# Optimization experiments

Hardware: AMD Instinct MI355X
Metric: run time of the kernel (lower is better)

The kernel has to match this reference:

```python
import jax, jax.numpy as jnp
import numpy as np

NH = 8      # num_heads
NP_ = 4     # num_points

def setup_inputs() -> dict:
    key = jax.random.key(0)
    ks = jax.random.split(key, 12)
    B, N, C = 8, 4096, 256
    query = jax.random.normal(ks[0], (B, N, C), jnp.float32)
    value = jax.random.normal(ks[1], (B, N, C), jnp.float32)
    reference_points = jax.random.uniform(ks[2], (B, N, 2), jnp.float32)
    xav = lambda k, i, o: jax.random.normal(k, (i, o), jnp.float32) * np.sqrt(2.0 / (i + o)).astype(np.float32)
    W_off = jax.random.normal(ks[3], (C, NH * NP_ * 2), jnp.float32) * 0.02  # small offsets (orig inits to 0)
    b_off = jax.random.normal(ks[4], (NH * NP_ * 2,), jnp.float32) * 0.02
    W_attn = xav(ks[5], C, NH * NP_)
    b_attn = jnp.zeros((NH * NP_,), jnp.float32)
    W_val = xav(ks[6], C, C)
    b_val = jnp.zeros((C,), jnp.float32)
    W_out = xav(ks[7], C, C)
    b_out = jnp.zeros((C,), jnp.float32)
    return dict(query=query, value=value, reference_points=reference_points,
                W_off=W_off, b_off=b_off, W_attn=W_attn, b_attn=b_attn,
                W_val=W_val, b_val=b_val, W_out=W_out, b_out=b_out)

def _deform_attn(query, value, reference_points, W_off, b_off, W_attn, b_attn, W_val, b_val, W_out, b_out):
    B, N, C = query.shape
    HW = value.shape[1]
    H = W = int(np.sqrt(HW))  # static
    hd = C // NH
    # value projection -> [B, NH, H*W, hd]
    vals = (value @ W_val + b_val).reshape(B, H, W, NH, hd)
    vals = vals.transpose(0, 3, 1, 2, 4).reshape(B, NH, H * W, hd)
    # offsets [B,N,NH,P,2] in [-0.5,0.5]; attention weights softmax over P
    off = jnp.tanh((query @ W_off + b_off).reshape(B, N, NH, NP_, 2)) * 0.5
    attn = jax.nn.softmax((query @ W_attn + b_attn).reshape(B, N, NH, NP_), axis=-1)
    # sampling locations in [0,1], then grid coords in [-1,1] (x=width, y=height)
    loc = jnp.clip(reference_points[:, :, None, None, :] + off, 0.0, 1.0)
    g = loc * 2.0 - 1.0
    # torch grid_sample, align_corners=False: pixel = (g+1)*size/2 - 0.5
    x = (g[..., 0] + 1.0) * (W * 0.5) - 0.5
    y = (g[..., 1] + 1.0) * (H * 0.5) - 0.5
    x0f = jnp.floor(x); y0f = jnp.floor(y)
    wx1 = x - x0f; wx0 = 1.0 - wx1
    wy1 = y - y0f; wy0 = 1.0 - wy1
    x0 = x0f.astype(jnp.int32); x1 = x0 + 1
    y0 = y0f.astype(jnp.int32); y1 = y0 + 1

    def corner(xi, yi, w):  # xi,yi,w: [B,N,NH,P]; zero padding outside
        valid = (xi >= 0) & (xi < W) & (yi >= 0) & (yi < H)
        idx = jnp.clip(yi, 0, H - 1) * W + jnp.clip(xi, 0, W - 1)
        idx_h = idx.transpose(0, 2, 1, 3).reshape(B, NH, N * NP_)      # [B,NH,N*P]
        gat = jnp.take_along_axis(vals, idx_h[..., None], axis=2)      # [B,NH,N*P,hd]
        wv = jnp.where(valid, w, 0.0).transpose(0, 2, 1, 3).reshape(B, NH, N * NP_)
        return gat * wv[..., None]

    sampled = (corner(x0, y0, wx0 * wy0) + corner(x1, y0, wx1 * wy0)
               + corner(x0, y1, wx0 * wy1) + corner(x1, y1, wx1 * wy1))
    sampled = sampled.reshape(B, NH, N, NP_, hd)
    attn_h = attn.transpose(0, 2, 1, 3)                                 # [B,NH,N,P]
    out = jnp.einsum('bhnpd,bhnp->bnhd', sampled, attn_h).reshape(B, N, C)
    return out @ W_out + b_out  # dropout is identity in eval

def reference(query, value, reference_points, W_off, b_off, W_attn, b_attn, W_val, b_val, W_out, b_out):
    return _deform_attn(query, value, reference_points, W_off, b_off, W_attn, b_attn, W_val, b_val, W_out, b_out)
```

## Files before the change

### kernel.cpp

```cpp
#include <hip/hip_runtime.h>
#include <math.h>

#define NHEAD 8
#define NPT 4
#define HDIM 32
#define IMG 64
#define CDIM 256
#define NQ 4096
#define BATCH 8
#define MTOT (BATCH * NQ)

typedef __attribute__((ext_vector_type(8))) short bf16x8;
typedef __attribute__((ext_vector_type(4))) float f32x4;

__device__ __forceinline__ unsigned short f2b(float f) {
    union { float f; unsigned u; } v; v.f = f;
    unsigned r = (v.u + 0x7FFFu + ((v.u >> 16) & 1u)) >> 16;
    return (unsigned short)r;
}
__device__ __forceinline__ float b2f(unsigned short u) {
    union { unsigned u; float f; } v; v.u = ((unsigned)u) << 16;
    return v.f;
}

#define SWZ(row, col)   ((col) ^ (((row) & 7) << 3))

__device__ __forceinline__ void gload16(const void* src, void* ldsbase) {
    __builtin_amdgcn_global_load_lds(
        (const __attribute__((address_space(1))) void*)src,
        (__attribute__((address_space(3))) void*)ldsbase, 16, 0, 0);
}


__global__ __launch_bounds__(256)
void cvt_weights_kernel(const float* __restrict__ Wv, const float* __restrict__ Wo,
                        const float* __restrict__ Woff, const float* __restrict__ Wattn,
                        const float* __restrict__ boff, const float* __restrict__ battn,
                        unsigned short* __restrict__ Wv_t, unsigned short* __restrict__ Wo_t,
                        unsigned short* __restrict__ Wl_h, unsigned short* __restrict__ Wl_l,
                        float* __restrict__ bias_lin)
{
    int tid = blockIdx.x * 256 + threadIdx.x;
    int n = tid & 255, k = tid >> 8;
    Wv_t[n * 256 + k] = f2b(Wv[k * 256 + n]);
    Wo_t[n * 256 + k] = f2b(Wo[k * 256 + n]);
    if (tid < 128 * 256) {
        int nn = tid >> 8;
        int kk = tid & 255;
        float v = (nn < 64) ? Woff[kk * 64 + nn]
                : (nn < 96) ? Wattn[kk * 32 + (nn - 64)] : 0.f;
        unsigned short hi = f2b(v);
        unsigned short lo = f2b(v - b2f(hi));
        Wl_h[nn * 256 + kk] = hi;
        Wl_l[nn * 256 + kk] = lo;
    }
    if (tid < 128)
        bias_lin[tid] = (tid < 64) ? boff[tid] : (tid < 96) ? battn[tid - 64] : 0.f;
}

__global__ __launch_bounds__(256)
void fused_gemms_kernel(const float* __restrict__ value,
                        const float* __restrict__ query,
                        const unsigned short* __restrict__ Wv_t,
                        const unsigned short* __restrict__ Wl_h,
                        const unsigned short* __restrict__ Wl_l,
                        const float* __restrict__ b_val,
                        unsigned short* __restrict__ projv,
                        float* __restrict__ lin)
{
    __shared__ __align__(16) char smem[32768];

    const int tid  = threadIdx.x;
    const int lane = tid & 63;
    const int wid  = tid >> 6;
    const int wr = (wid >> 1) * 64;
    const int wc = (wid & 1) * 64;
    const int l15 = lane & 15;
    const int lk  = (lane >> 4) * 8;

    const int b = blockIdx.x & 7;
    const int j = blockIdx.x >> 3;

    f32x4 acc[4][4];
    #pragma unroll
    for (int m = 0; m < 4; ++m)
        #pragma unroll
        for (int n = 0; n < 4; ++n)
            #pragma unroll
            for (int r = 0; r < 4; ++r) acc[m][n][r] = 0.f;

    if (j < 64) {
        unsigned short (*As)[64] = (unsigned short(*)[64])smem;
        unsigned short (*Bs)[64] = (unsigned short(*)[64])(smem + 16384);
        const int gm = (b << 12) + ((j & 31) << 7);
        const int gn = (j >> 5) << 7;
        const int rl  = lane >> 3;
        const int ch  = (lane & 7) ^ rl;

        for (int k0 = 0; k0 < 256; k0 += 64) {
            #pragma unroll
            for (int it = 0; it < 4; ++it) {
                const int br = it * 32 + wid * 8;
                gload16(&Wv_t[(size_t)(gn + br + rl) * 256 + k0 + ch * 8], &Bs[br][0]);
            }
            #pragma unroll
            for (int it = 0; it < 4; ++it) {
                const int chunk = it * 256 + tid;
                const int row = chunk >> 3;
                const int kc  = (chunk & 7) << 3;
                const float4* src = (const float4*)&value[(size_t)(gm + row) * 256 + k0 + kc];
                const float4 a = src[0], bb = src[1];
                float f[8] = {a.x, a.y, a.z, a.w, bb.x, bb.y, bb.z, bb.w};
                unsigned short h[8];
                #pragma unroll
                for (int jj = 0; jj < 8; ++jj) h[jj] = f2b(f[jj]);
                *(uint4*)&As[row][SWZ(row, kc)] = *(const uint4*)h;
            }
            __syncthreads();

            #pragma unroll
            for (int kk = 0; kk < 64; kk += 32) {
                bf16x8 a[4], bv[4];
                #pragma unroll
                for (int m = 0; m < 4; ++m) {
                    const int r = wr + m * 16 + l15;
                    a[m] = *(const bf16x8*)&As[r][SWZ(r, kk + lk)];
                }
                #pragma unroll
                for (int n = 0; n < 4; ++n) {
                    const int r = wc + n * 16 + l15;
                    bv[n] = *(const bf16x8*)&Bs[r][SWZ(r, kk + lk)];
                }
                #pragma unroll
                for (int m = 0; m < 4; ++m)
                    #pragma unroll
                    for (int n = 0; n < 4; ++n)
                        acc[m][n] = __builtin_amdgcn_mfma_f32_16x16x32_bf16(a[m], bv[n], acc[m][n], 0, 0, 0);
            }
            __syncthreads();
        }

        const int cr = (lane >> 4) * 4;
        #pragma unroll
        for (int n = 0; n < 4; ++n) {
            const int col = gn + wc + n * 16 + l15;
            const float bvv = b_val[col];
            #pragma unroll
            for (int m = 0; m < 4; ++m)
                #pragma unroll
                for (int r = 0; r < 4; ++r) {
                    const int row = gm + wr + m * 16 + cr + r;
                    projv[(size_t)row * 256 + col] = f2b(acc[m][n][r] + bvv);
                }
        }
    } else {
        float (*Aq)[32] = (float(*)[32])smem;
        unsigned short (*Bh)[32] = (unsigned short(*)[32])(smem + 16384);
        unsigned short (*Bl)[32] = (unsigned short(*)[32])(smem + 24576);
        const int u  = j - 64;
        const int gm = (b << 12) + ((u & 31) << 7);
        const int kq = u >> 5;
        const int rla = lane >> 3;
        const int ca  = (lane & 7) ^ rla;
        const int rsb = lane >> 2;
        const int cb  = (lane & 3) ^ (rsb & 3);

        for (int k0 = kq * 128; k0 < kq * 128 + 128; k0 += 32) {
            #pragma unroll
            for (int i = 0; i < 4; ++i) {
                const int ar = wid * 32 + i * 8;
                gload16(&query[(size_t)(gm + ar + rla) * 256 + k0 + ca * 4], &Aq[ar][0]);
            }
            #pragma unroll
            for (int i = 0; i < 2; ++i) {
                const int br = wid * 32 + i * 16;
                gload16(&Wl_h[(size_t)(br + rsb) * 256 + k0 + cb * 8], &Bh[br][0]);
                gload16(&Wl_l[(size_t)(br + rsb) * 256 + k0 + cb * 8], &Bl[br][0]);
            }
            __syncthreads();

            bf16x8 ah[4], al[4];
            #pragma unroll
            for (int m = 0; m < 4; ++m) {
                const int r = wr + m * 16 + l15;
                const int c0 = ((lk >> 2) ^ (r & 7)) << 2;
                const int c1 = (((lk >> 2) + 1) ^ (r & 7)) << 2;
                const f32x4 qa = *(const f32x4*)&Aq[r][c0];
                const f32x4 qb = *(const f32x4*)&Aq[r][c1];
                float f[8] = {qa.x, qa.y, qa.z, qa.w, qb.x, qb.y, qb.z, qb.w};
                unsigned short h[8], l[8];
                #pragma unroll
                for (int jj = 0; jj < 8; ++jj) {
                    h[jj] = f2b(f[jj]);
                    l[jj] = f2b(f[jj] - b2f(h[jj]));
                }
                ah[m] = *(const bf16x8*)h;
                al[m] = *(const bf16x8*)l;
            }

            const int nN = (wc == 0) ? 4 : 2;
            #pragma unroll
            for (int n = 0; n < 4; ++n) {
                if (n >= nN) break;
                const int r = wc + n * 16 + l15;
                const int c = ((lk >> 3) ^ (r & 3)) << 3;
                const bf16x8 bh = *(const bf16x8*)&Bh[r][c];
                const bf16x8 bl = *(const bf16x8*)&Bl[r][c];
                #pragma unroll
                for (int m = 0; m < 4; ++m) {
                    acc[m][n] = __builtin_amdgcn_mfma_f32_16x16x32_bf16(ah[m], bh, acc[m][n], 0, 0, 0);
                    acc[m][n] = __builtin_amdgcn_mfma_f32_16x16x32_bf16(ah[m], bl, acc[m][n], 0, 0, 0);
                    acc[m][n] = __builtin_amdgcn_mfma_f32_16x16x32_bf16(al[m], bh, acc[m][n], 0, 0, 0);
                }
            }
            __syncthreads();
        }

        float* dst = lin + (size_t)kq * MTOT * 96;
        const int cr = (lane >> 4) * 4;
        #pragma unroll
        for (int n = 0; n < 4; ++n) {
            const int col = wc + n * 16 + l15;
            if (col < 96) {
                #pragma unroll
                for (int m = 0; m < 4; ++m)
                    #pragma unroll
                    for (int r = 0; r < 4; ++r) {
                        const int row = gm + wr + m * 16 + cr + r;
                        dst[(size_t)row * 96 + col] = acc[m][n][r];
                    }
            }
        }
    }
}

__global__ __launch_bounds__(256)
void gemm_out_kernel(const unsigned short* __restrict__ Ap,
                     const unsigned short* __restrict__ Bt,
                     const float* __restrict__ bias,
                     float* __restrict__ C)
{
    __shared__ unsigned short As[128][64];
    __shared__ unsigned short Bs[128][64];

    const int tid  = threadIdx.x;
    const int lane = tid & 63;
    const int wid  = tid >> 6;
    const int gm = ((blockIdx.x & 7) << 12) + ((blockIdx.x >> 3) << 7);
    const int gn = blockIdx.y * 128;
    const int wr = (wid >> 1) * 64;
    const int wc = (wid & 1) * 64;
    const int l15 = lane & 15;
    const int lk  = (lane >> 4) * 8;
    const int rl  = lane >> 3;
    const int ch  = (lane & 7) ^ rl;

    f32x4 acc[4][4];
    #pragma unroll
    for (int m = 0; m < 4; ++m)
        #pragma unroll
        for (int n = 0; n < 4; ++n)
            #pragma unroll
            for (int r = 0; r < 4; ++r) acc[m][n][r] = 0.f;

    for (int k0 = 0; k0 < 256; k0 += 64) {
        #pragma unroll
        for (int it = 0; it < 4; ++it) {
            const int br = it * 32 + wid * 8;
            gload16(&Bt[(size_t)(gn + br + rl) * 256 + k0 + ch * 8], &Bs[br][0]);
            gload16(&Ap[(size_t)(gm + br + rl) * 256 + k0 + ch * 8], &As[br][0]);
        }
        __syncthreads();

        #pragma unroll
        for (int kk = 0; kk < 64; kk += 32) {
            bf16x8 a[4], b[4];
            #pragma unroll
            for (int m = 0; m < 4; ++m) {
                const int r = wr + m * 16 + l15;
                a[m] = *(const bf16x8*)&As[r][SWZ(r, kk + lk)];
            }
            #pragma unroll
            for (int n = 0; n < 4; ++n) {
                const int r = wc + n * 16 + l15;
                b[n] = *(const bf16x8*)&Bs[r][SWZ(r, kk + lk)];
            }
            #pragma unroll
            for (int m = 0; m < 4; ++m)
                #pragma unroll
                for (int n = 0; n < 4; ++n)
                    acc[m][n] = __builtin_amdgcn_mfma_f32_16x16x32_bf16(a[m], b[n], acc[m][n], 0, 0, 0);
        }
        __syncthreads();
    }

    const int cr = (lane >> 4) * 4;
    #pragma unroll
    for (int n = 0; n < 4; ++n) {
        const int col = gn + wc + n * 16 + l15;
        const float bv = bias[col];
        #pragma unroll
        for (int m = 0; m < 4; ++m)
            #pragma unroll
            for (int r = 0; r < 4; ++r) {
                const int row = gm + wr + m * 16 + cr + r;
                C[(size_t)row * 256 + col] = acc[m][n][r] + bv;
            }
    }
}

__global__ __launch_bounds__(256)
void sample_gather_kernel(const unsigned short* __restrict__ projv,
                          const float* __restrict__ lin,
                          const float* __restrict__ bias_lin,
                          const float* __restrict__ refp,
                          unsigned short* __restrict__ sampled)
{
    __shared__ float4 s_w[8][32];
    __shared__ unsigned s_xy[8][32];

    const int i = blockIdx.x;
    const int b = i & 7;
    const int bn0 = (b << 12) + ((i >> 3) << 3);
    const int t = threadIdx.x;

    {
        const int sub = t >> 5;
        const int q = t & 31;
        const int h = q >> 2;
        const int p = q & 3;
        const int bn = bn0 + sub;
        const float2 rp = *(const float2*)&refp[(size_t)bn * 2];
        const size_t base0 = (size_t)bn * 96;
        const size_t base1 = (size_t)MTOT * 96 + base0;
        const float2 o0 = *(const float2*)&lin[base0 + h * 8 + p * 2];
        const float2 o1 = *(const float2*)&lin[base1 + h * 8 + p * 2];
        const float2 ob = *(const float2*)&bias_lin[h * 8 + p * 2];
        const float olx = o0.x + o1.x + ob.x;
        const float oly = o0.y + o1.y + ob.y;
        const float al  = lin[base0 + 64 + q] + lin[base1 + 64 + q] + bias_lin[64 + q];

        float mx = al;
        mx = fmaxf(mx, __shfl_xor(mx, 1));
        mx = fmaxf(mx, __shfl_xor(mx, 2));
        float e = expf(al - mx);
        float s = e;
        s += __shfl_xor(s, 1);
        s += __shfl_xor(s, 2);
        const float aw = e / s;

        const float lx = fminf(fmaxf(rp.x + tanhf(olx) * 0.5f, 0.f), 1.f);
        const float ly = fminf(fmaxf(rp.y + tanhf(oly) * 0.5f, 0.f), 1.f);
        const float x = lx * (float)IMG - 0.5f;
        const float y = ly * (float)IMG - 0.5f;
        const float x0f = floorf(x), y0f = floorf(y);
        const int x0 = (int)x0f, y0 = (int)y0f;
        const float wx1 = x - x0f, wx0 = 1.f - wx1;
        const float wy1 = y - y0f, wy0 = 1.f - wy1;
        const bool vx0 = (x0 >= 0), vx1 = (x0 + 1 < IMG);
        const bool vy0 = (y0 >= 0), vy1 = (y0 + 1 < IMG);
        float4 w;
        w.x = (vx0 && vy0) ? wx0 * wy0 * aw : 0.f;
        w.y = (vx1 && vy0) ? wx1 * wy0 * aw : 0.f;
        w.z = (vx0 && vy1) ? wx0 * wy1 * aw : 0.f;
        w.w = (vx1 && vy1) ? wx1 * wy1 * aw : 0.f;
        const int x0c = min(max(x0, 0), IMG - 1), x1c = min(max(x0 + 1, 0), IMG - 1);
        const int y0c = min(max(y0, 0), IMG - 1), y1c = min(max(y0 + 1, 0), IMG - 1);
        s_w[sub][q] = w;
        s_xy[sub][q] = (unsigned)x0c | ((unsigned)x1c << 8) | ((unsigned)y0c << 16) | ((unsigned)y1c << 24);
    }
    __syncthreads();

    const int l = t & 63;
    const int h2 = l >> 3;
    const int cp = l & 7;
    const unsigned short* vbase = projv + ((size_t)b << 20) + h2 * HDIM + cp * 4;

    #pragma unroll
    for (int pass = 0; pass < 2; ++pass) {
        const int sub = (t >> 6) + pass * 4;
        const int bn = bn0 + sub;

        float a0 = 0.f, a1 = 0.f, a2 = 0.f, a3 = 0.f;
        #pragma unroll
        for (int p = 0; p < 4; ++p) {
            const float4 w = s_w[sub][h2 * 4 + p];
            const unsigned xy = s_xy[sub][h2 * 4 + p];
            const int x0 = xy & 255, x1 = (xy >> 8) & 255;
            const int y0 = (xy >> 16) & 255, y1 = xy >> 24;
            const uint2 u00 = *(const uint2*)&vbase[(((y0 << 6) + x0) << 8)];
            const uint2 u01 = *(const uint2*)&vbase[(((y0 << 6) + x1) << 8)];
            const uint2 u10 = *(const uint2*)&vbase[(((y1 << 6) + x0) << 8)];
            const uint2 u11 = *(const uint2*)&vbase[(((y1 << 6) + x1) << 8)];
            a0 += w.x * b2f((unsigned short)(u00.x & 0xffff)) + w.y * b2f((unsigned short)(u01.x & 0xffff))
                + w.z * b2f((unsigned short)(u10.x & 0xffff)) + w.w * b2f((unsigned short)(u11.x & 0xffff));
            a1 += w.x * b2f((unsigned short)(u00.x >> 16)) + w.y * b2f((unsigned short)(u01.x >> 16))
                + w.z * b2f((unsigned short)(u10.x >> 16)) + w.w * b2f((unsigned short)(u11.x >> 16));
            a2 += w.x * b2f((unsigned short)(u00.y & 0xffff)) + w.y * b2f((unsigned short)(u01.y & 0xffff))
                + w.z * b2f((unsigned short)(u10.y & 0xffff)) + w.w * b2f((unsigned short)(u11.y & 0xffff));
            a3 += w.x * b2f((unsigned short)(u00.y >> 16)) + w.y * b2f((unsigned short)(u01.y >> 16))
                + w.z * b2f((unsigned short)(u10.y >> 16)) + w.w * b2f((unsigned short)(u11.y >> 16));
        }
        uint2 outp;
        outp.x = (unsigned)f2b(a0) | ((unsigned)f2b(a1) << 16);
        outp.y = (unsigned)f2b(a2) | ((unsigned)f2b(a3) << 16);
        *(uint2*)&sampled[(size_t)bn * 256 + h2 * HDIM + cp * 4] = outp;
    }
}

extern "C" void kernel_launch(void* const* d_in, const int* in_sizes, int n_in,
                              void* d_out, int out_size, void* d_ws, size_t ws_size,
                              hipStream_t stream)
{
    const float* query  = (const float*)d_in[0];
    const float* value  = (const float*)d_in[1];
    const float* refp   = (const float*)d_in[2];
    const float* W_off  = (const float*)d_in[3];
    const float* b_off  = (const float*)d_in[4];
    const float* W_attn = (const float*)d_in[5];
    const float* b_attn = (const float*)d_in[6];
    const float* W_val  = (const float*)d_in[7];
    const float* b_val  = (const float*)d_in[8];
    const float* W_out  = (const float*)d_in[9];
    const float* b_out  = (const float*)d_in[10];
    float* out = (float*)d_out;

    char* ws = (char*)d_ws;
    unsigned short* projv    = (unsigned short*)ws; ws += (size_t)MTOT * 256 * 2;
    unsigned short* sampled  = (unsigned short*)ws; ws += (size_t)MTOT * 256 * 2;
    float*          lin      = (float*)ws;          ws += (size_t)2 * MTOT * 96 * 4;
    unsigned short* Wv_t     = (unsigned short*)ws; ws += 256 * 256 * 2;
    unsigned short* Wo_t     = (unsigned short*)ws; ws += 256 * 256 * 2;
    unsigned short* Wl_h     = (unsigned short*)ws; ws += 128 * 256 * 2;
    unsigned short* Wl_l     = (unsigned short*)ws; ws += 128 * 256 * 2;
    float*          bias_lin = (float*)ws;          ws += 128 * 4;

    dim3 blk(256);

    cvt_weights_kernel<<<dim3(256), blk, 0, stream>>>(W_val, W_out, W_off, W_attn, b_off, b_attn,
                                                      Wv_t, Wo_t, Wl_h, Wl_l, bias_lin);

    fused_gemms_kernel<<<dim3(1024), blk, 0, stream>>>(value, query, Wv_t, Wl_h, Wl_l,
                                                       b_val, projv, lin);

    sample_gather_kernel<<<dim3(MTOT / 8), blk, 0, stream>>>(projv, lin, bias_lin, refp, sampled);

    gemm_out_kernel<<<dim3(MTOT / 128, 2), blk, 0, stream>>>(sampled, Wo_t, b_out, out);
}
```

Baseline: 70.15 us.

## Double-buffer value-projection and output GEMMs with software-pipelined K loop

Replaces the single-buffered 64-wide K loop of the value-projection and output GEMMs with a shared templated body that uses two 32-wide K stages in LDS. The next stage's global loads (async LDS loads for bf16 operands, register prefetch for fp32 value) are issued before computing the current stage, with explicit vmcnt waits and barriers. The aim is to hide global memory latency behind MFMA work. It adds hand-written waitcnt bookkeeping that must match the number of outstanding loads, and it doubles the number of barrier rounds.

```diff
diff --git a/kernel.cpp b/kernel.cpp
--- a/kernel.cpp
+++ b/kernel.cpp
@@ -23,13 +23,19 @@
     return v.f;
 }
 
-#define SWZ(row, col)   ((col) ^ (((row) & 7) << 3))
-
 __device__ __forceinline__ void gload16(const void* src, void* ldsbase) {
     __builtin_amdgcn_global_load_lds(
         (const __attribute__((address_space(1))) void*)src,
         (__attribute__((address_space(3))) void*)ldsbase, 16, 0, 0);
 }
+
+#define VMCNT0() asm volatile("s_waitcnt vmcnt(0)" ::: "memory")
+#define VMCNT2() asm volatile("s_waitcnt vmcnt(2)" ::: "memory")
+#define VMCNT4() asm volatile("s_waitcnt vmcnt(4)" ::: "memory")
+#define VMCNT6() asm volatile("s_waitcnt vmcnt(6)" ::: "memory")
+#define LGKM0()  asm volatile("s_waitcnt lgkmcnt(0)" ::: "memory")
+#define BAR()    __builtin_amdgcn_s_barrier()
+#define SCHEDB() __builtin_amdgcn_sched_barrier(0)
 
 
 __global__ __launch_bounds__(256)
@@ -58,6 +64,145 @@
         bias_lin[tid] = (tid < 64) ? boff[tid] : (tid < 96) ? battn[tid - 64] : 0.f;
 }
 
+template<bool A_F32, bool OUT_BF16>
+__device__ void gemm_pipe_body(char* smem,
+                               const void* __restrict__ Ap,
+                               const unsigned short* __restrict__ Bt,
+                               const float* __restrict__ bias,
+                               void* __restrict__ C,
+                               int gm, int gn, int tid)
+{
+    unsigned short (*As)[128][32] = (unsigned short(*)[128][32])smem;
+    unsigned short (*Bs)[128][32] = (unsigned short(*)[128][32])(smem + 16384);
+
+    const int lane = tid & 63, wid = tid >> 6;
+    const int wr = (wid >> 1) * 64, wc = (wid & 1) * 64;
+    const int l15 = lane & 15;
+    const int lc  = lane >> 4;
+    const int r16 = lane >> 2;
+    const int cb  = (lane & 3) ^ (r16 & 3);
+
+    float fa[2][8];
+
+    f32x4 acc[4][4];
+    #pragma unroll
+    for (int m = 0; m < 4; ++m)
+        #pragma unroll
+        for (int n = 0; n < 4; ++n)
+            #pragma unroll
+            for (int r = 0; r < 4; ++r) acc[m][n][r] = 0.f;
+
+    auto stageB = [&](int s, int k0) {
+        #pragma unroll
+        for (int i = 0; i < 2; ++i) {
+            const int br = wid * 32 + i * 16;
+            gload16(&Bt[(size_t)(gn + br + r16) * 256 + k0 + cb * 8], &Bs[s][br][0]);
+        }
+    };
+    auto stageA_gl = [&](int s, int k0) {
+        #pragma unroll
+        for (int i = 0; i < 2; ++i) {
+            const int br = wid * 32 + i * 16;
+            gload16(&((const unsigned short*)Ap)[(size_t)(gm + br + r16) * 256 + k0 + cb * 8], &As[s][br][0]);
+        }
+    };
+    auto loadA_regs = [&](int k0) {
+        #pragma unroll
+        for (int it = 0; it < 2; ++it) {
+            const int chunk = it * 256 + tid;
+            const int row = chunk >> 2;
+            const int kc  = (chunk & 3) << 3;
+            const float4* src = (const float4*)&((const float*)Ap)[(size_t)(gm + row) * 256 + k0 + kc];
+            const float4 a = src[0], b = src[1];
+            fa[it][0] = a.x; fa[it][1] = a.y; fa[it][2] = a.z; fa[it][3] = a.w;
+            fa[it][4] = b.x; fa[it][5] = b.y; fa[it][6] = b.z; fa[it][7] = b.w;
+        }
+    };
+    auto writeA = [&](int s) {
+        #pragma unroll
+        for (int it = 0; it < 2; ++it) {
+            const int chunk = it * 256 + tid;
+            const int row = chunk >> 2;
+            const int kc  = (chunk & 3) << 3;
+            unsigned short h[8];
+            #pragma unroll
+            for (int j = 0; j < 8; ++j) h[j] = f2b(fa[it][j]);
+            const int pc = (((kc >> 3) ^ (row & 3)) << 3);
+            *(uint4*)&As[s][row][pc] = *(const uint4*)h;
+        }
+    };
+    auto compute = [&](int s) {
+        bf16x8 a[4], b[4];
+        #pragma unroll
+        for (int m = 0; m < 4; ++m) {
+            const int r = wr + m * 16 + l15;
+            a[m] = *(const bf16x8*)&As[s][r][((lc ^ (r & 3)) << 3)];
+        }
+        #pragma unroll
+        for (int n = 0; n < 4; ++n) {
+            const int r = wc + n * 16 + l15;
+            b[n] = *(const bf16x8*)&Bs[s][r][((lc ^ (r & 3)) << 3)];
+        }
+        #pragma unroll
+        for (int m = 0; m < 4; ++m)
+            #pragma unroll
+            for (int n = 0; n < 4; ++n)
+                acc[m][n] = __builtin_amdgcn_mfma_f32_16x16x32_bf16(a[m], b[n], acc[m][n], 0, 0, 0);
+    };
+
+    if (A_F32) {
+        loadA_regs(0);
+        stageB(0, 0);
+        VMCNT2(); SCHEDB();
+        writeA(0);
+    } else {
+        stageA_gl(0, 0);
+        stageB(0, 0);
+    }
+
+    int c = 0;
+    #pragma unroll
+    for (int k = 0; k < 8; ++k) {
+        if (k < 7) {
+            if (A_F32) loadA_regs((k + 1) * 32);
+            else       stageA_gl(c ^ 1, (k + 1) * 32);
+            stageB(c ^ 1, (k + 1) * 32);
+            if (A_F32) { VMCNT6(); } else { VMCNT4(); }
+        } else {
+            VMCNT0();
+        }
+        SCHEDB();
+        LGKM0();
+        BAR();
+        compute(c);
+        if (k < 7 && A_F32) {
+            VMCNT2(); SCHEDB();
+            writeA(c ^ 1);
+        }
+        LGKM0();
+        BAR();
+        c ^= 1;
+    }
+
+    const int cr = (lane >> 4) * 4;
+    #pragma unroll
+    for (int n = 0; n < 4; ++n) {
+        const int col = gn + wc + n * 16 + l15;
+        const float bv = bias[col];
+        #pragma unroll
+        for (int m = 0; m < 4; ++m)
+            #pragma unroll
+            for (int r = 0; r < 4; ++r) {
+                const int row = gm + wr + m * 16 + cr + r;
+                const float v = acc[m][n][r] + bv;
+                if (OUT_BF16)
+                    ((unsigned short*)C)[(size_t)row * 256 + col] = f2b(v);
+                else
+                    ((float*)C)[(size_t)row * 256 + col] = v;
+            }
+    }
+}
+
 __global__ __launch_bounds__(256)
 void fused_gemms_kernel(const float* __restrict__ value,
                         const float* __restrict__ query,
@@ -73,13 +218,30 @@
     const int tid  = threadIdx.x;
     const int lane = tid & 63;
     const int wid  = tid >> 6;
+    const int b = blockIdx.x & 7;
+    const int j = blockIdx.x >> 3;
+
+    if (j < 64) {
+        gemm_pipe_body<true, true>(smem, value, Wv_t, b_val, projv,
+                                   (b << 12) + ((j & 31) << 7), (j >> 5) << 7, tid);
+        return;
+    }
+
     const int wr = (wid >> 1) * 64;
     const int wc = (wid & 1) * 64;
     const int l15 = lane & 15;
     const int lk  = (lane >> 4) * 8;
 
-    const int b = blockIdx.x & 7;
-    const int j = blockIdx.x >> 3;
+    float (*Aq)[32] = (float(*)[32])smem;
+    unsigned short (*Bh)[32] = (unsigned short(*)[32])(smem + 16384);
+    unsigned short (*Bl)[32] = (unsigned short(*)[32])(smem + 24576);
+    const int u  = j - 64;
+    const int gm = (b << 12) + ((u & 31) << 7);
+    const int kq = u >> 5;
+    const int rla = lane >> 3;
+    const int ca  = (lane & 7) ^ rla;
+    const int rsb = lane >> 2;
+    const int cb  = (lane & 3) ^ (rsb & 3);
 
     f32x4 acc[4][4];
     #pragma unroll
@@ -89,147 +251,70 @@
             #pragma unroll
             for (int r = 0; r < 4; ++r) acc[m][n][r] = 0.f;
 
-    if (j < 64) {
-        unsigned short (*As)[64] = (unsigned short(*)[64])smem;
-        unsigned short (*Bs)[64] = (unsigned short(*)[64])(smem + 16384);
-        const int gm = (b << 12) + ((j & 31) << 7);
-        const int gn = (j >> 5) << 7;
-        const int rl  = lane >> 3;
-        const int ch  = (lane & 7) ^ rl;
-
-        for (int k0 = 0; k0 < 256; k0 += 64) {
-            #pragma unroll
-            for (int it = 0; it < 4; ++it) {
-                const int br = it * 32 + wid * 8;
-                gload16(&Wv_t[(size_t)(gn + br + rl) * 256 + k0 + ch * 8], &Bs[br][0]);
+    for (int k0 = kq * 128; k0 < kq * 128 + 128; k0 += 32) {
+        #pragma unroll
+        for (int i = 0; i < 4; ++i) {
+            const int ar = wid * 32 + i * 8;
+            gload16(&query[(size_t)(gm + ar + rla) * 256 + k0 + ca * 4], &Aq[ar][0]);
+        }
+        #pragma unroll
+        for (int i = 0; i < 2; ++i) {
+            const int br = wid * 32 + i * 16;
+            gload16(&Wl_h[(size_t)(br + rsb) * 256 + k0 + cb * 8], &Bh[br][0]);
+            gload16(&Wl_l[(size_t)(br + rsb) * 256 + k0 + cb * 8], &Bl[br][0]);
+        }
+        __syncthreads();
+
+        bf16x8 ah[4], al[4];
+        #pragma unroll
+        for (int m = 0; m < 4; ++m) {
+            const int r = wr + m * 16 + l15;
+            const int c0 = ((lk >> 2) ^ (r & 7)) << 2;
+            const int c1 = (((lk >> 2) + 1) ^ (r & 7)) << 2;
+            const f32x4 qa = *(const f32x4*)&Aq[r][c0];
+            const f32x4 qb = *(const f32x4*)&Aq[r][c1];
+            float f[8] = {qa.x, qa.y, qa.z, qa.w, qb.x, qb.y, qb.z, qb.w};
+            unsigned short h[8], l[8];
+            #pragma unroll
+            for (int jj = 0; jj < 8; ++jj) {
+                h[jj] = f2b(f[jj]);
+                l[jj] = f2b(f[jj] - b2f(h[jj]));
             }
-            #pragma unroll
-            for (int it = 0; it < 4; ++it) {
-                const int chunk = it * 256 + tid;
-                const int row = chunk >> 3;
-                const int kc  = (chunk & 7) << 3;
-                const float4* src = (const float4*)&value[(size_t)(gm + row) * 256 + k0 + kc];
-                const float4 a = src[0], bb = src[1];
-                float f[8] = {a.x, a.y, a.z, a.w, bb.x, bb.y, bb.z, bb.w};
-                unsigned short h[8];
-                #pragma unroll
-                for (int jj = 0; jj < 8; ++jj) h[jj] = f2b(f[jj]);
-                *(uint4*)&As[row][SWZ(row, kc)] = *(const uint4*)h;
+            ah[m] = *(const bf16x8*)h;
+            al[m] = *(const bf16x8*)l;
+        }
+
+        const int nN = (wc == 0) ? 4 : 2;
+        #pragma unroll
+        for (int n = 0; n < 4; ++n) {
+            if (n >= nN) break;
+            const int r = wc + n * 16 + l15;
+            const int c = ((lk >> 3) ^ (r & 3)) << 3;
+            const bf16x8 bh = *(const bf16x8*)&Bh[r][c];
+            const bf16x8 bl = *(const bf16x8*)&Bl[r][c];
+            #pragma unroll
+            for (int m = 0; m < 4; ++m) {
+                acc[m][n] = __builtin_amdgcn_mfma_f32_16x16x32_bf16(ah[m], bh, acc[m][n], 0, 0, 0);
+                acc[m][n] = __builtin_amdgcn_mfma_f32_16x16x32_bf16(ah[m], bl, acc[m][n], 0, 0, 0);
+                acc[m][n] = __builtin_amdgcn_mfma_f32_16x16x32_bf16(al[m], bh, acc[m][n], 0, 0, 0);
             }
-            __syncthreads();
-
-            #pragma unroll
-            for (int kk = 0; kk < 64; kk += 32) {
-                bf16x8 a[4], bv[4];
-                #pragma unroll
-                for (int m = 0; m < 4; ++m) {
-                    const int r = wr + m * 16 + l15;
-                    a[m] = *(const bf16x8*)&As[r][SWZ(r, kk + lk)];
-                }
-                #pragma unroll
-                for (int n = 0; n < 4; ++n) {
-                    const int r = wc + n * 16 + l15;
-                    bv[n] = *(const bf16x8*)&Bs[r][SWZ(r, kk + lk)];
-                }
-                #pragma unroll
-                for (int m = 0; m < 4; ++m)
-                    #pragma unroll
-                    for (int n = 0; n < 4; ++n)
-                        acc[m][n] = __builtin_amdgcn_mfma_f32_16x16x32_bf16(a[m], bv[n], acc[m][n], 0, 0, 0);
-            }
-            __syncthreads();
-        }
-
-        const int cr = (lane >> 4) * 4;
-        #pragma unroll
-        for (int n = 0; n < 4; ++n) {
-            const int col = gn + wc + n * 16 + l15;
-            const float bvv = b_val[col];
+        }
+        __syncthreads();
+    }
+
+    float* dst = lin + (size_t)kq * MTOT * 96;
+    const int cr = (lane >> 4) * 4;
+    #pragma unroll
+    for (int n = 0; n < 4; ++n) {
+        const int col = wc + n * 16 + l15;
+        if (col < 96) {
             #pragma unroll
             for (int m = 0; m < 4; ++m)
                 #pragma unroll
                 for (int r = 0; r < 4; ++r) {
                     const int row = gm + wr + m * 16 + cr + r;
-                    projv[(size_t)row * 256 + col] = f2b(acc[m][n][r] + bvv);
+                    dst[(size_t)row * 96 + col] = acc[m][n][r];
                 }
-        }
-    } else {
-        float (*Aq)[32] = (float(*)[32])smem;
-        unsigned short (*Bh)[32] = (unsigned short(*)[32])(smem + 16384);
-        unsigned short (*Bl)[32] = (unsigned short(*)[32])(smem + 24576);
-        const int u  = j - 64;
-        const int gm = (b << 12) + ((u & 31) << 7);
-        const int kq = u >> 5;
-        const int rla = lane >> 3;
-        const int ca  = (lane & 7) ^ rla;
-        const int rsb = lane >> 2;
-        const int cb  = (lane & 3) ^ (rsb & 3);
-
-        for (int k0 = kq * 128; k0 < kq * 128 + 128; k0 += 32) {
-            #pragma unroll
-            for (int i = 0; i < 4; ++i) {
-                const int ar = wid * 32 + i * 8;
-                gload16(&query[(size_t)(gm + ar + rla) * 256 + k0 + ca * 4], &Aq[ar][0]);
-            }
-            #pragma unroll
-            for (int i = 0; i < 2; ++i) {
-                const int br = wid * 32 + i * 16;
-                gload16(&Wl_h[(size_t)(br + rsb) * 256 + k0 + cb * 8], &Bh[br][0]);
-                gload16(&Wl_l[(size_t)(br + rsb) * 256 + k0 + cb * 8], &Bl[br][0]);
-            }
-            __syncthreads();
-
-            bf16x8 ah[4], al[4];
-            #pragma unroll
-            for (int m = 0; m < 4; ++m) {
-                const int r = wr + m * 16 + l15;
-                const int c0 = ((lk >> 2) ^ (r & 7)) << 2;
-                const int c1 = (((lk >> 2) + 1) ^ (r & 7)) << 2;
-                const f32x4 qa = *(const f32x4*)&Aq[r][c0];
-                const f32x4 qb = *(const f32x4*)&Aq[r][c1];
-                float f[8] = {qa.x, qa.y, qa.z, qa.w, qb.x, qb.y, qb.z, qb.w};
-                unsigned short h[8], l[8];
-                #pragma unroll
-                for (int jj = 0; jj < 8; ++jj) {
-                    h[jj] = f2b(f[jj]);
-                    l[jj] = f2b(f[jj] - b2f(h[jj]));
-                }
-                ah[m] = *(const bf16x8*)h;
-                al[m] = *(const bf16x8*)l;
-            }
-
-            const int nN = (wc == 0) ? 4 : 2;
-            #pragma unroll
-            for (int n = 0; n < 4; ++n) {
-                if (n >= nN) break;
-                const int r = wc + n * 16 + l15;
-                const int c = ((lk >> 3) ^ (r & 3)) << 3;
-                const bf16x8 bh = *(const bf16x8*)&Bh[r][c];
-                const bf16x8 bl = *(const bf16x8*)&Bl[r][c];
-                #pragma unroll
-                for (int m = 0; m < 4; ++m) {
-                    acc[m][n] = __builtin_amdgcn_mfma_f32_16x16x32_bf16(ah[m], bh, acc[m][n], 0, 0, 0);
-                    acc[m][n] = __builtin_amdgcn_mfma_f32_16x16x32_bf16(ah[m], bl, acc[m][n], 0, 0, 0);
-                    acc[m][n] = __builtin_amdgcn_mfma_f32_16x16x32_bf16(al[m], bh, acc[m][n], 0, 0, 0);
-                }
-            }
-            __syncthreads();
-        }
-
-        float* dst = lin + (size_t)kq * MTOT * 96;
-        const int cr = (lane >> 4) * 4;
-        #pragma unroll
-        for (int n = 0; n < 4; ++n) {
-            const int col = wc + n * 16 + l15;
-            if (col < 96) {
-                #pragma unroll
-                for (int m = 0; m < 4; ++m)
-                    #pragma unroll
-                    for (int r = 0; r < 4; ++r) {
-                        const int row = gm + wr + m * 16 + cr + r;
-                        dst[(size_t)row * 96 + col] = acc[m][n][r];
-                    }
-            }
         }
     }
 }
@@ -240,73 +325,10 @@
                      const float* __restrict__ bias,
                      float* __restrict__ C)
 {
-    __shared__ unsigned short As[128][64];
-    __shared__ unsigned short Bs[128][64];
-
-    const int tid  = threadIdx.x;
-    const int lane = tid & 63;
-    const int wid  = tid >> 6;
+    __shared__ __align__(16) char smem[32768];
     const int gm = ((blockIdx.x & 7) << 12) + ((blockIdx.x >> 3) << 7);
     const int gn = blockIdx.y * 128;
-    const int wr = (wid >> 1) * 64;
-    const int wc = (wid & 1) * 64;
-    const int l15 = lane & 15;
-    const int lk  = (lane >> 4) * 8;
-    const int rl  = lane >> 3;
-    const int ch  = (lane & 7) ^ rl;
-
-    f32x4 acc[4][4];
-    #pragma unroll
-    for (int m = 0; m < 4; ++m)
-        #pragma unroll
-        for (int n = 0; n < 4; ++n)
-            #pragma unroll
-            for (int r = 0; r < 4; ++r) acc[m][n][r] = 0.f;
-
-    for (int k0 = 0; k0 < 256; k0 += 64) {
-        #pragma unroll
-        for (int it = 0; it < 4; ++it) {
-            const int br = it * 32 + wid * 8;
-            gload16(&Bt[(size_t)(gn + br + rl) * 256 + k0 + ch * 8], &Bs[br][0]);
-            gload16(&Ap[(size_t)(gm + br + rl) * 256 + k0 + ch * 8], &As[br][0]);
-        }
-        __syncthreads();
-
-        #pragma unroll
-        for (int kk = 0; kk < 64; kk += 32) {
-            bf16x8 a[4], b[4];
-            #pragma unroll
-            for (int m = 0; m < 4; ++m) {
-                const int r = wr + m * 16 + l15;
-                a[m] = *(const bf16x8*)&As[r][SWZ(r, kk + lk)];
-            }
-            #pragma unroll
-            for (int n = 0; n < 4; ++n) {
-                const int r = wc + n * 16 + l15;
-                b[n] = *(const bf16x8*)&Bs[r][SWZ(r, kk + lk)];
-            }
-            #pragma unroll
-            for (int m = 0; m < 4; ++m)
-                #pragma unroll
-                for (int n = 0; n < 4; ++n)
-                    acc[m][n] = __builtin_amdgcn_mfma_f32_16x16x32_bf16(a[m], b[n], acc[m][n], 0, 0, 0);
-        }
-        __syncthreads();
-    }
-
-    const int cr = (lane >> 4) * 4;
-    #pragma unroll
-    for (int n = 0; n < 4; ++n) {
-        const int col = gn + wc + n * 16 + l15;
-        const float bv = bias[col];
-        #pragma unroll
-        for (int m = 0; m < 4; ++m)
-            #pragma unroll
-            for (int r = 0; r < 4; ++r) {
-                const int row = gm + wr + m * 16 + cr + r;
-                C[(size_t)row * 256 + col] = acc[m][n][r] + bv;
-            }
-    }
+    gemm_pipe_body<false, false>(smem, Ap, Bt, bias, C, gm, gn, threadIdx.x);
 }
 
 __global__ __launch_bounds__(256)
```

Measured after the change: 68.66 us (median of 2 runs). -2.1%, faster.
